# Performance work log

Measured on AMD Instinct MI355X. Metric: run time of the kernel, lower is better.

## Reference

```python
import jax, jax.numpy as jnp
import numpy as np

B, N, D = 1024, 128, 512
TEMP = 0.5          # temperature
DECAY = 0.98        # protection_decay


def setup_inputs() -> dict:
    key = jax.random.key(0)
    ks = jax.random.split(key, 16)
    s = 0.02
    return {
        "hidden": jax.random.normal(ks[0], (B, D), jnp.float32),
        "working_keys": jax.random.normal(ks[1], (B, N, D), jnp.float32),
        "working_values": jax.random.normal(ks[2], (B, N, D), jnp.float32),
        "working_protection": jax.random.uniform(ks[3], (B, N), jnp.float32),
        "working_usage": jax.random.uniform(ks[4], (B, N), jnp.float32),
        "working_age": jax.random.uniform(ks[5], (B, N), jnp.float32),
        "Wk": jax.random.normal(ks[6], (D, D), jnp.float32) * s,
        "bk": jnp.zeros((D,), jnp.float32),
        "Wv": jax.random.normal(ks[7], (D, D), jnp.float32) * s,
        "bv": jnp.zeros((D,), jnp.float32),
        "Wwr": jax.random.normal(ks[8], (D, 1), jnp.float32) * s,
        "bwr": jnp.zeros((1,), jnp.float32),
        "Wmg": jax.random.normal(ks[9], (D, 1), jnp.float32) * s,
        "bmg": jnp.zeros((1,), jnp.float32),
        "Wbd": jax.random.normal(ks[10], (D, 1), jnp.float32) * s,
        "bbd": jnp.zeros((1,), jnp.float32),
        "Wim": jax.random.normal(ks[11], (D, 1), jnp.float32) * s,
        "bim": jnp.zeros((1,), jnp.float32),
        "Woc": jax.random.normal(ks[12], (D, 1), jnp.float32) * s,
        "boc": jnp.zeros((1,), jnp.float32),
        "Wpr": jax.random.normal(ks[13], (D, 1), jnp.float32) * s,
        "bpr": jnp.zeros((1,), jnp.float32),
    }


def _normalize(x, eps=1e-6):
    # matches torch F.normalize: x / max(||x||, eps)
    n = jnp.linalg.norm(x, axis=-1, keepdims=True)
    return x / jnp.maximum(n, eps)


def reference(hidden, working_keys, working_values, working_protection,
              working_usage, working_age,
              Wk, bk, Wv, bv, Wwr, bwr, Wmg, bmg, Wbd, bbd,
              Wim, bim, Woc, boc, Wpr, bpr):
    candidate_key = jnp.tanh(hidden @ Wk + bk)              # [B,D]
    candidate_value = jnp.tanh(hidden @ Wv + bv)            # [B,D]
    write_strength = jax.nn.sigmoid(hidden @ Wwr + bwr)     # [B,1]
    importance = jax.nn.sigmoid(hidden @ Wim + bim)         # [B,1]

    norm_candidate = _normalize(candidate_key)
    norm_keys = _normalize(working_keys)
    similarity = jnp.einsum('bd,bnd->bn', norm_candidate, norm_keys)  # [B,N]

    norm_occupancy = jnp.clip(
        jnp.linalg.norm(working_values, axis=-1) / (working_values.shape[-1] ** 0.5), 0.0, 1.0)
    learned_occupancy = jax.nn.sigmoid(working_values @ Woc + boc)[..., 0]  # [B,N]
    occupancy = jnp.clip(0.5 * learned_occupancy + 0.5 * norm_occupancy, 0.0, 1.0)
    learned_protection = jax.nn.sigmoid(working_values @ Wpr + bpr)[..., 0]
    effective_protection = jnp.clip(0.4 * learned_protection + 0.6 * working_protection, 0.0, 1.0)
    effective_usage = jnp.clip(0.5 * occupancy + 0.5 * working_usage, 0.0, 1.0)
    effective_age = jnp.clip(working_age, 0.0, 1.0)

    merge_weights = jax.nn.softmax(similarity / TEMP, axis=-1)
    replace_scores = (1.15 * (1.0 - occupancy) + 0.85 * (1.0 - effective_protection)
                      + 0.65 * effective_age + 0.45 * (1.0 - effective_usage)
                      + 0.25 * (1.0 - similarity))
    replace_weights = jax.nn.softmax(replace_scores / TEMP, axis=-1)

    merge_index = jnp.argmax(merge_weights, axis=-1)      # [B]
    replace_index = jnp.argmax(replace_weights, axis=-1)  # [B]
    gi = merge_index[:, None]
    max_similarity = jnp.take_along_axis(similarity, gi, axis=1)        # [B,1]
    matched_occupancy = jnp.take_along_axis(occupancy, gi, axis=1)
    matched_usage = jnp.take_along_axis(effective_usage, gi, axis=1)
    matched_age = jnp.take_along_axis(effective_age, gi, axis=1)

    merge_preference = jax.nn.sigmoid((hidden @ Wmg + bmg) + 2.4 * max_similarity
                                      + 1.6 * (matched_occupancy - 0.5)
                                      + 1.0 * (matched_usage - 0.5)
                                      - 0.8 * matched_age)                # [B,1]
    merge_candidate = (max_similarity > 0.55) & (matched_occupancy > 0.35)  # [B,1]
    use_merge = (merge_preference >= 0.5) & merge_candidate                 # [B,1]

    target_index = jnp.where(use_merge[:, 0], merge_index, replace_index)  # [B]
    target_weights = jax.nn.one_hot(target_index, N, dtype=hidden.dtype)   # [B,N]

    binding_strength = jax.nn.sigmoid((hidden @ Wbd + bbd) + 2.2 * max_similarity)  # [B,1]
    conflict = jnp.clip(1.0 - similarity, 0.0, 1.0)
    overwrite = (0.15 + 0.85 * write_strength) * target_weights * (1.0 - 0.65 * effective_protection * conflict)  # [B,N]
    ow = overwrite[..., None]                 # [B,N,1]

    um = use_merge[:, :, None]                # [B,1,1]
    bs = binding_strength[:, :, None]         # [B,1,1]
    im = importance[:, :, None]               # [B,1,1]
    key_mix = jnp.where(um, 0.22 + 0.38 * bs, 0.78 + 0.18 * bs)
    value_mix = jnp.where(um, 0.45 + 0.35 * im, 0.75 + 0.2 * im)

    updated_keys = working_keys + ow * key_mix * (candidate_key[:, None, :] - working_keys)
    updated_values = working_values + ow * value_mix * (candidate_value[:, None, :] - working_values)

    protection_boost = overwrite * (0.5 + 0.5 * importance)
    updated_protection = jnp.clip(working_protection * DECAY + protection_boost, 0.0, 1.0)

    # stats flattened to a tuple (same order as the torch dict)
    return (updated_keys, updated_values, updated_protection,
            write_strength[:, 0], merge_preference[:, 0], binding_strength[:, 0],
            overwrite.mean(axis=-1), updated_protection.mean(axis=-1),
            max_similarity[:, 0], overwrite)
```

## Files before the change

### kernel.cpp

```cpp
#include <hip/hip_runtime.h>
#include <math.h>

#define BATCH 1024
#define NSLOT 128
#define DDIM  512
#define BB 8

__device__ __forceinline__ float sigmoidf_(float x) { return 1.0f / (1.0f + expf(-x)); }
__device__ __forceinline__ float clip01(float x) { return fminf(fmaxf(x, 0.0f), 1.0f); }
__device__ __forceinline__ float dot4(float4 a, float4 b) {
    return fmaf(a.x, b.x, fmaf(a.y, b.y, fmaf(a.z, b.z, a.w * b.w)));
}

__global__ __launch_bounds__(256) void k_gemm(
    const float* __restrict__ hidden,
    const float* __restrict__ Wk, const float* __restrict__ bk,
    const float* __restrict__ Wv, const float* __restrict__ bv,
    float* __restrict__ ck, float* __restrict__ cv)
{
    __shared__ float hs[BB][DDIM];
    const int b0 = blockIdx.x * BB;
    const int c = blockIdx.y * 256 + threadIdx.x;
    for (int i = threadIdx.x; i < BB * DDIM; i += 256)
        hs[i / DDIM][i % DDIM] = hidden[(size_t)b0 * DDIM + i];
    __syncthreads();

    float ak[BB], av[BB];
#pragma unroll
    for (int bb = 0; bb < BB; ++bb) { ak[bb] = 0.f; av[bb] = 0.f; }

#pragma unroll 4
    for (int e = 0; e < DDIM; ++e) {
        const float wk = Wk[(size_t)e * DDIM + c];
        const float wv = Wv[(size_t)e * DDIM + c];
#pragma unroll
        for (int bb = 0; bb < BB; ++bb) {
            ak[bb] = fmaf(hs[bb][e], wk, ak[bb]);
            av[bb] = fmaf(hs[bb][e], wv, av[bb]);
        }
    }
    const float bkc = bk[c], bvc = bv[c];
#pragma unroll
    for (int bb = 0; bb < BB; ++bb) {
        ck[(size_t)(b0 + bb) * DDIM + c] = tanhf(ak[bb] + bkc);
        cv[(size_t)(b0 + bb) * DDIM + c] = tanhf(av[bb] + bvc);
    }
}

__global__ __launch_bounds__(64) void k_scal(
    const float* __restrict__ hidden, const float* __restrict__ ck,
    const float* __restrict__ Wwr, const float* __restrict__ bwr,
    const float* __restrict__ Wmg, const float* __restrict__ bmg,
    const float* __restrict__ Wbd, const float* __restrict__ bbd,
    const float* __restrict__ Wim, const float* __restrict__ bim,
    float* __restrict__ scal)
{
    const int b = blockIdx.x;
    const int lane = threadIdx.x;
    const float4* h4 = (const float4*)(hidden + (size_t)b * DDIM);
    const float4* c4 = (const float4*)(ck + (size_t)b * DDIM);
    const float4* wr4 = (const float4*)Wwr;
    const float4* mg4 = (const float4*)Wmg;
    const float4* bd4 = (const float4*)Wbd;
    const float4* im4 = (const float4*)Wim;

    float dwr = 0.f, dmg = 0.f, dbd = 0.f, dim = 0.f, css = 0.f;
#pragma unroll
    for (int i = 0; i < 2; ++i) {
        const int idx = lane + i * 64;
        const float4 h = h4[idx];
        const float4 c = c4[idx];
        dwr += dot4(h, wr4[idx]);
        dmg += dot4(h, mg4[idx]);
        dbd += dot4(h, bd4[idx]);
        dim += dot4(h, im4[idx]);
        css += dot4(c, c);
    }
#pragma unroll
    for (int off = 32; off > 0; off >>= 1) {
        dwr += __shfl_down(dwr, off, 64);
        dmg += __shfl_down(dmg, off, 64);
        dbd += __shfl_down(dbd, off, 64);
        dim += __shfl_down(dim, off, 64);
        css += __shfl_down(css, off, 64);
    }
    if (lane == 0) {
        scal[b * 5 + 0] = sigmoidf_(dwr + bwr[0]);
        scal[b * 5 + 1] = sigmoidf_(dim + bim[0]);
        scal[b * 5 + 2] = dmg + bmg[0];
        scal[b * 5 + 3] = dbd + bbd[0];
        scal[b * 5 + 4] = 1.0f / fmaxf(sqrtf(css), 1e-6f);
    }
}

__global__ __launch_bounds__(256) void k_stream(
    const float* __restrict__ wkeys, const float* __restrict__ wvals,
    const float* __restrict__ wprot,
    const float* __restrict__ ck, const float* __restrict__ scal,
    const float* __restrict__ Woc, const float* __restrict__ boc,
    const float* __restrict__ Wpr, const float* __restrict__ bpr,
    float* __restrict__ out_keys, float* __restrict__ out_vals,
    float* __restrict__ sim_ws, float* __restrict__ occ_ws, float* __restrict__ epr_ws)
{
    const int wave = threadIdx.x >> 6;
    const int lane = threadIdx.x & 63;
    const size_t r = (size_t)blockIdx.x * 4 + wave;
    const int b = (int)(r >> 7);
    const float4* k4 = (const float4*)wkeys + r * (DDIM / 4);
    const float4* v4 = (const float4*)wvals + r * (DDIM / 4);
    const float4* c4 = (const float4*)ck + (size_t)b * (DDIM / 4);
    const float4* oc4 = (const float4*)Woc;
    const float4* pr4 = (const float4*)Wpr;
    float4* ok4 = (float4*)out_keys + r * (DDIM / 4);
    float4* ov4 = (float4*)out_vals + r * (DDIM / 4);

    float dk = 0.f, kk = 0.f, vv = 0.f, doc = 0.f, dpr = 0.f;
#pragma unroll
    for (int i = 0; i < 2; ++i) {
        const int idx = lane + i * 64;
        const float4 k = k4[idx];
        const float4 c = c4[idx];
        const float4 v = v4[idx];
        dk  += dot4(k, c);
        kk  += dot4(k, k);
        vv  += dot4(v, v);
        doc += dot4(v, oc4[idx]);
        dpr += dot4(v, pr4[idx]);
        ok4[idx] = k;
        ov4[idx] = v;
    }
#pragma unroll
    for (int off = 32; off > 0; off >>= 1) {
        dk  += __shfl_down(dk, off, 64);
        kk  += __shfl_down(kk, off, 64);
        vv  += __shfl_down(vv, off, 64);
        doc += __shfl_down(doc, off, 64);
        dpr += __shfl_down(dpr, off, 64);
    }
    if (lane == 0) {
        const float inv_ck = scal[b * 5 + 4];
        const float sim = dk * inv_ck * (1.0f / fmaxf(sqrtf(kk), 1e-6f));
        const float nocc = clip01(sqrtf(vv) * 0.04419417382415922f);
        const float locc = sigmoidf_(doc + boc[0]);
        const float occ = clip01(0.5f * locc + 0.5f * nocc);
        const float lpr = sigmoidf_(dpr + bpr[0]);
        const float epr = clip01(0.4f * lpr + 0.6f * wprot[r]);
        sim_ws[r] = sim;
        occ_ws[r] = occ;
        epr_ws[r] = epr;
    }
}

__global__ __launch_bounds__(128) void k_final(
    const float* __restrict__ wkeys, const float* __restrict__ wvals,
    const float* __restrict__ wprot, const float* __restrict__ wusage,
    const float* __restrict__ wage,
    const float* __restrict__ ck, const float* __restrict__ cv,
    const float* __restrict__ sim_ws, const float* __restrict__ occ_ws,
    const float* __restrict__ epr_ws, const float* __restrict__ scal,
    float* __restrict__ out_keys, float* __restrict__ out_vals,
    float* __restrict__ out_prot, float* __restrict__ out_wstr,
    float* __restrict__ out_mpref, float* __restrict__ out_bstr,
    float* __restrict__ out_ovmean, float* __restrict__ out_pmean,
    float* __restrict__ out_msim, float* __restrict__ out_ovr)
{
    const int b = blockIdx.x;
    const int n = threadIdx.x;
    __shared__ float s_sim[NSLOT], s_rs[NSLOT], s_occ[NSLOT], s_eu[NSLOT],
                     s_ea[NSLOT], s_ep[NSLOT], s_up[NSLOT];
    __shared__ int s_idx[2];

    const size_t r = (size_t)b * NSLOT + n;
    const float sim = sim_ws[r];
    const float occ = occ_ws[r];
    const float ep  = epr_ws[r];
    const float eu  = clip01(0.5f * occ + 0.5f * wusage[r]);
    const float ea  = clip01(wage[r]);
    const float rs  = 1.15f * (1.f - occ) + 0.85f * (1.f - ep) + 0.65f * ea
                    + 0.45f * (1.f - eu) + 0.25f * (1.f - sim);
    s_sim[n] = sim; s_rs[n] = rs; s_occ[n] = occ;
    s_eu[n] = eu;   s_ea[n] = ea; s_ep[n] = ep;
    __syncthreads();

    if (n == 0) {
        int mi = 0, ri = 0;
        float mv = s_sim[0], rv = s_rs[0];
        for (int i = 1; i < NSLOT; ++i) {
            if (s_sim[i] > mv) { mv = s_sim[i]; mi = i; }
            if (s_rs[i]  > rv) { rv = s_rs[i];  ri = i; }
        }
        s_idx[0] = mi; s_idx[1] = ri;
    }
    __syncthreads();

    const int mi = s_idx[0], ri = s_idx[1];
    const float max_sim = s_sim[mi];
    const float m_occ = s_occ[mi], m_eu = s_eu[mi], m_ea = s_ea[mi];
    const float wstr = scal[b * 5 + 0];
    const float imv  = scal[b * 5 + 1];
    const float mgl  = scal[b * 5 + 2];
    const float bdl  = scal[b * 5 + 3];

    const float mpref = sigmoidf_(mgl + 2.4f * max_sim + 1.6f * (m_occ - 0.5f)
                                  + 1.0f * (m_eu - 0.5f) - 0.8f * m_ea);
    const bool mcand = (max_sim > 0.55f) && (m_occ > 0.35f);
    const bool use_merge = (mpref >= 0.5f) && mcand;
    const int target = use_merge ? mi : ri;
    const float bstr = sigmoidf_(bdl + 2.2f * max_sim);

    const float conflict_t = clip01(1.f - s_sim[target]);
    const float ov = (0.15f + 0.85f * wstr) * (1.f - 0.65f * s_ep[target] * conflict_t);
    const float ovn = (n == target) ? ov : 0.f;
    out_ovr[r] = ovn;

    const float pb = ovn * (0.5f + 0.5f * imv);
    const float up = clip01(wprot[r] * 0.98f + pb);
    out_prot[r] = up;
    s_up[n] = up;
    __syncthreads();

    if (n == 0) {
        float s = 0.f;
        for (int i = 0; i < NSLOT; ++i) s += s_up[i];
        out_wstr[b]   = wstr;
        out_mpref[b]  = mpref;
        out_bstr[b]   = bstr;
        out_ovmean[b] = ov * (1.0f / NSLOT);
        out_pmean[b]  = s * (1.0f / NSLOT);
        out_msim[b]   = max_sim;
    }

    const float kmix = use_merge ? (0.22f + 0.38f * bstr) : (0.78f + 0.18f * bstr);
    const float vmix = use_merge ? (0.45f + 0.35f * imv)  : (0.75f + 0.20f * imv);
    const float fk = ov * kmix;
    const float fv = ov * vmix;
    const size_t base = ((size_t)b * NSLOT + target) * DDIM;
    const float4* wk4 = (const float4*)(wkeys + base);
    const float4* wv4 = (const float4*)(wvals + base);
    const float4* ck4 = (const float4*)(ck + (size_t)b * DDIM);
    const float4* cv4 = (const float4*)(cv + (size_t)b * DDIM);
    float4* ok4 = (float4*)(out_keys + base);
    float4* ov4 = (float4*)(out_vals + base);

    const float4 k = wk4[n], c = ck4[n];
    const float4 v = wv4[n], w = cv4[n];
    float4 nk, nv;
    nk.x = fmaf(fk, c.x - k.x, k.x); nk.y = fmaf(fk, c.y - k.y, k.y);
    nk.z = fmaf(fk, c.z - k.z, k.z); nk.w = fmaf(fk, c.w - k.w, k.w);
    nv.x = fmaf(fv, w.x - v.x, v.x); nv.y = fmaf(fv, w.y - v.y, v.y);
    nv.z = fmaf(fv, w.z - v.z, v.z); nv.w = fmaf(fv, w.w - v.w, v.w);
    ok4[n] = nk;
    ov4[n] = nv;
}

extern "C" void kernel_launch(void* const* d_in, const int* in_sizes, int n_in,
                              void* d_out, int out_size, void* d_ws, size_t ws_size,
                              hipStream_t stream)
{
    (void)in_sizes; (void)n_in; (void)out_size; (void)ws_size;

    const float* hidden = (const float*)d_in[0];
    const float* wkeys  = (const float*)d_in[1];
    const float* wvals  = (const float*)d_in[2];
    const float* wprot  = (const float*)d_in[3];
    const float* wusage = (const float*)d_in[4];
    const float* wage   = (const float*)d_in[5];
    const float* Wk  = (const float*)d_in[6];
    const float* bk  = (const float*)d_in[7];
    const float* Wv  = (const float*)d_in[8];
    const float* bv  = (const float*)d_in[9];
    const float* Wwr = (const float*)d_in[10];
    const float* bwr = (const float*)d_in[11];
    const float* Wmg = (const float*)d_in[12];
    const float* bmg = (const float*)d_in[13];
    const float* Wbd = (const float*)d_in[14];
    const float* bbd = (const float*)d_in[15];
    const float* Wim = (const float*)d_in[16];
    const float* bim = (const float*)d_in[17];
    const float* Woc = (const float*)d_in[18];
    const float* boc = (const float*)d_in[19];
    const float* Wpr = (const float*)d_in[20];
    const float* bpr = (const float*)d_in[21];

    float* out = (float*)d_out;
    const size_t BND = (size_t)BATCH * NSLOT * DDIM;
    const size_t BN  = (size_t)BATCH * NSLOT;
    float* out_keys   = out;
    float* out_vals   = out_keys + BND;
    float* out_prot   = out_vals + BND;
    float* out_wstr   = out_prot + BN;
    float* out_mpref  = out_wstr + BATCH;
    float* out_bstr   = out_mpref + BATCH;
    float* out_ovmean = out_bstr + BATCH;
    float* out_pmean  = out_ovmean + BATCH;
    float* out_msim   = out_pmean + BATCH;
    float* out_ovr    = out_msim + BATCH;

    float* ws  = (float*)d_ws;
    float* ck  = ws;
    float* cv  = ck + (size_t)BATCH * DDIM;
    float* simw = cv + (size_t)BATCH * DDIM;
    float* occw = simw + BN;
    float* eprw = occw + BN;
    float* scal = eprw + BN;

    k_gemm<<<dim3(BATCH / BB, 2), 256, 0, stream>>>(hidden, Wk, bk, Wv, bv, ck, cv);
    k_scal<<<BATCH, 64, 0, stream>>>(hidden, ck, Wwr, bwr, Wmg, bmg, Wbd, bbd,
                                     Wim, bim, scal);
    k_stream<<<(BATCH * NSLOT) / 4, 256, 0, stream>>>(
        wkeys, wvals, wprot, ck, scal, Woc, boc, Wpr, bpr,
        out_keys, out_vals, simw, occw, eprw);
    k_final<<<BATCH, NSLOT, 0, stream>>>(
        wkeys, wvals, wprot, wusage, wage, ck, cv, simw, occw, eprw, scal,
        out_keys, out_vals, out_prot, out_wstr, out_mpref, out_bstr,
        out_ovmean, out_pmean, out_msim, out_ovr);
}
```

Baseline: 1.112 ms.

## Fuse four kernels into prep and main kernels with per-batch slot streaming

Merges the GEMM and the scalar-projection kernel into one prep kernel that computes the gate dot products and candidate-key norms from the tile already in registers and shared memory. Merges the streaming similarity pass and the final selection into one per-batch kernel, which removes the sim/occ/protection workspace round-trips and two launches. Replaces the serial argmax with wave shuffle reductions. The prep kernel now uses 4 batch rows per block and 512 threads, which lowers weight reuse per block.

```diff
diff --git a/kernel.cpp b/kernel.cpp
--- a/kernel.cpp
+++ b/kernel.cpp
@@ -4,7 +4,7 @@
 #define BATCH 1024
 #define NSLOT 128
 #define DDIM  512
-#define BB 8
+#define BB 4
 
 __device__ __forceinline__ float sigmoidf_(float x) { return 1.0f / (1.0f + expf(-x)); }
 __device__ __forceinline__ float clip01(float x) { return fminf(fmaxf(x, 0.0f), 1.0f); }
@@ -12,152 +12,90 @@
     return fmaf(a.x, b.x, fmaf(a.y, b.y, fmaf(a.z, b.z, a.w * b.w)));
 }
 
-__global__ __launch_bounds__(256) void k_gemm(
+__global__ __launch_bounds__(512) void k_prep(
     const float* __restrict__ hidden,
     const float* __restrict__ Wk, const float* __restrict__ bk,
     const float* __restrict__ Wv, const float* __restrict__ bv,
-    float* __restrict__ ck, float* __restrict__ cv)
+    const float* __restrict__ Wwr, const float* __restrict__ bwr,
+    const float* __restrict__ Wmg, const float* __restrict__ bmg,
+    const float* __restrict__ Wbd, const float* __restrict__ bbd,
+    const float* __restrict__ Wim, const float* __restrict__ bim,
+    float* __restrict__ ck, float* __restrict__ cv, float* __restrict__ scal)
 {
-    __shared__ float hs[BB][DDIM];
+    __shared__ __align__(16) float hs[BB][DDIM];
+    __shared__ float sred[8][BB * 5];
     const int b0 = blockIdx.x * BB;
-    const int c = blockIdx.y * 256 + threadIdx.x;
-    for (int i = threadIdx.x; i < BB * DDIM; i += 256)
-        hs[i / DDIM][i % DDIM] = hidden[(size_t)b0 * DDIM + i];
-    __syncthreads();
-
-    float ak[BB], av[BB];
-#pragma unroll
-    for (int bb = 0; bb < BB; ++bb) { ak[bb] = 0.f; av[bb] = 0.f; }
-
+    const int c  = threadIdx.x;
+
+    {
+        const float4* h4 = (const float4*)(hidden + (size_t)b0 * DDIM);
+        ((float4*)&hs[0][0])[c] = h4[c];
+    }
+    __syncthreads();
+
+    float ak[BB] = {0.f, 0.f, 0.f, 0.f}, av[BB] = {0.f, 0.f, 0.f, 0.f};
 #pragma unroll 4
     for (int e = 0; e < DDIM; ++e) {
         const float wk = Wk[(size_t)e * DDIM + c];
         const float wv = Wv[(size_t)e * DDIM + c];
 #pragma unroll
         for (int bb = 0; bb < BB; ++bb) {
-            ak[bb] = fmaf(hs[bb][e], wk, ak[bb]);
-            av[bb] = fmaf(hs[bb][e], wv, av[bb]);
-        }
-    }
+            const float h = hs[bb][e];
+            ak[bb] = fmaf(h, wk, ak[bb]);
+            av[bb] = fmaf(h, wv, av[bb]);
+        }
+    }
+
     const float bkc = bk[c], bvc = bv[c];
+    const float wwr = Wwr[c], wmg = Wmg[c], wbd = Wbd[c], wim = Wim[c];
+    float p[BB * 5];
 #pragma unroll
     for (int bb = 0; bb < BB; ++bb) {
-        ck[(size_t)(b0 + bb) * DDIM + c] = tanhf(ak[bb] + bkc);
-        cv[(size_t)(b0 + bb) * DDIM + c] = tanhf(av[bb] + bvc);
-    }
-}
-
-__global__ __launch_bounds__(64) void k_scal(
-    const float* __restrict__ hidden, const float* __restrict__ ck,
-    const float* __restrict__ Wwr, const float* __restrict__ bwr,
-    const float* __restrict__ Wmg, const float* __restrict__ bmg,
-    const float* __restrict__ Wbd, const float* __restrict__ bbd,
-    const float* __restrict__ Wim, const float* __restrict__ bim,
-    float* __restrict__ scal)
-{
-    const int b = blockIdx.x;
-    const int lane = threadIdx.x;
-    const float4* h4 = (const float4*)(hidden + (size_t)b * DDIM);
-    const float4* c4 = (const float4*)(ck + (size_t)b * DDIM);
-    const float4* wr4 = (const float4*)Wwr;
-    const float4* mg4 = (const float4*)Wmg;
-    const float4* bd4 = (const float4*)Wbd;
-    const float4* im4 = (const float4*)Wim;
-
-    float dwr = 0.f, dmg = 0.f, dbd = 0.f, dim = 0.f, css = 0.f;
-#pragma unroll
-    for (int i = 0; i < 2; ++i) {
-        const int idx = lane + i * 64;
-        const float4 h = h4[idx];
-        const float4 c = c4[idx];
-        dwr += dot4(h, wr4[idx]);
-        dmg += dot4(h, mg4[idx]);
-        dbd += dot4(h, bd4[idx]);
-        dim += dot4(h, im4[idx]);
-        css += dot4(c, c);
-    }
-#pragma unroll
-    for (int off = 32; off > 0; off >>= 1) {
-        dwr += __shfl_down(dwr, off, 64);
-        dmg += __shfl_down(dmg, off, 64);
-        dbd += __shfl_down(dbd, off, 64);
-        dim += __shfl_down(dim, off, 64);
-        css += __shfl_down(css, off, 64);
-    }
-    if (lane == 0) {
-        scal[b * 5 + 0] = sigmoidf_(dwr + bwr[0]);
-        scal[b * 5 + 1] = sigmoidf_(dim + bim[0]);
-        scal[b * 5 + 2] = dmg + bmg[0];
-        scal[b * 5 + 3] = dbd + bbd[0];
-        scal[b * 5 + 4] = 1.0f / fmaxf(sqrtf(css), 1e-6f);
-    }
-}
-
-__global__ __launch_bounds__(256) void k_stream(
-    const float* __restrict__ wkeys, const float* __restrict__ wvals,
-    const float* __restrict__ wprot,
-    const float* __restrict__ ck, const float* __restrict__ scal,
-    const float* __restrict__ Woc, const float* __restrict__ boc,
-    const float* __restrict__ Wpr, const float* __restrict__ bpr,
-    float* __restrict__ out_keys, float* __restrict__ out_vals,
-    float* __restrict__ sim_ws, float* __restrict__ occ_ws, float* __restrict__ epr_ws)
-{
-    const int wave = threadIdx.x >> 6;
-    const int lane = threadIdx.x & 63;
-    const size_t r = (size_t)blockIdx.x * 4 + wave;
-    const int b = (int)(r >> 7);
-    const float4* k4 = (const float4*)wkeys + r * (DDIM / 4);
-    const float4* v4 = (const float4*)wvals + r * (DDIM / 4);
-    const float4* c4 = (const float4*)ck + (size_t)b * (DDIM / 4);
-    const float4* oc4 = (const float4*)Woc;
-    const float4* pr4 = (const float4*)Wpr;
-    float4* ok4 = (float4*)out_keys + r * (DDIM / 4);
-    float4* ov4 = (float4*)out_vals + r * (DDIM / 4);
-
-    float dk = 0.f, kk = 0.f, vv = 0.f, doc = 0.f, dpr = 0.f;
-#pragma unroll
-    for (int i = 0; i < 2; ++i) {
-        const int idx = lane + i * 64;
-        const float4 k = k4[idx];
-        const float4 c = c4[idx];
-        const float4 v = v4[idx];
-        dk  += dot4(k, c);
-        kk  += dot4(k, k);
-        vv  += dot4(v, v);
-        doc += dot4(v, oc4[idx]);
-        dpr += dot4(v, pr4[idx]);
-        ok4[idx] = k;
-        ov4[idx] = v;
-    }
-#pragma unroll
-    for (int off = 32; off > 0; off >>= 1) {
-        dk  += __shfl_down(dk, off, 64);
-        kk  += __shfl_down(kk, off, 64);
-        vv  += __shfl_down(vv, off, 64);
-        doc += __shfl_down(doc, off, 64);
-        dpr += __shfl_down(dpr, off, 64);
-    }
-    if (lane == 0) {
-        const float inv_ck = scal[b * 5 + 4];
-        const float sim = dk * inv_ck * (1.0f / fmaxf(sqrtf(kk), 1e-6f));
-        const float nocc = clip01(sqrtf(vv) * 0.04419417382415922f);
-        const float locc = sigmoidf_(doc + boc[0]);
-        const float occ = clip01(0.5f * locc + 0.5f * nocc);
-        const float lpr = sigmoidf_(dpr + bpr[0]);
-        const float epr = clip01(0.4f * lpr + 0.6f * wprot[r]);
-        sim_ws[r] = sim;
-        occ_ws[r] = occ;
-        epr_ws[r] = epr;
-    }
-}
-
-__global__ __launch_bounds__(128) void k_final(
+        const float k = tanhf(ak[bb] + bkc);
+        const float v = tanhf(av[bb] + bvc);
+        ck[(size_t)(b0 + bb) * DDIM + c] = k;
+        cv[(size_t)(b0 + bb) * DDIM + c] = v;
+        const float h = hs[bb][c];
+        p[bb * 5 + 0] = h * wwr;
+        p[bb * 5 + 1] = h * wim;
+        p[bb * 5 + 2] = h * wmg;
+        p[bb * 5 + 3] = h * wbd;
+        p[bb * 5 + 4] = k * k;
+    }
+#pragma unroll
+    for (int off = 32; off > 0; off >>= 1)
+#pragma unroll
+        for (int j = 0; j < BB * 5; ++j) p[j] += __shfl_down(p[j], off, 64);
+
+    const int wave = threadIdx.x >> 6, lane = threadIdx.x & 63;
+    if (lane == 0)
+#pragma unroll
+        for (int j = 0; j < BB * 5; ++j) sred[wave][j] = p[j];
+    __syncthreads();
+
+    if (threadIdx.x < BB * 5) {
+        float s = 0.f;
+#pragma unroll
+        for (int w = 0; w < 8; ++w) s += sred[w][threadIdx.x];
+        const int bb = threadIdx.x / 5, st = threadIdx.x % 5;
+        float outv;
+        if      (st == 0) outv = sigmoidf_(s + bwr[0]);
+        else if (st == 1) outv = sigmoidf_(s + bim[0]);
+        else if (st == 2) outv = s + bmg[0];
+        else if (st == 3) outv = s + bbd[0];
+        else              outv = 1.0f / fmaxf(sqrtf(s), 1e-6f);
+        scal[(b0 + bb) * 5 + st] = outv;
+    }
+}
+
+__global__ __launch_bounds__(512) void k_main(
     const float* __restrict__ wkeys, const float* __restrict__ wvals,
     const float* __restrict__ wprot, const float* __restrict__ wusage,
     const float* __restrict__ wage,
     const float* __restrict__ ck, const float* __restrict__ cv,
-    const float* __restrict__ sim_ws, const float* __restrict__ occ_ws,
-    const float* __restrict__ epr_ws, const float* __restrict__ scal,
+    const float* __restrict__ scal,
+    const float* __restrict__ Woc, const float* __restrict__ boc,
+    const float* __restrict__ Wpr, const float* __restrict__ bpr,
     float* __restrict__ out_keys, float* __restrict__ out_vals,
     float* __restrict__ out_prot, float* __restrict__ out_wstr,
     float* __restrict__ out_mpref, float* __restrict__ out_bstr,
@@ -165,92 +103,139 @@
     float* __restrict__ out_msim, float* __restrict__ out_ovr)
 {
     const int b = blockIdx.x;
-    const int n = threadIdx.x;
-    __shared__ float s_sim[NSLOT], s_rs[NSLOT], s_occ[NSLOT], s_eu[NSLOT],
-                     s_ea[NSLOT], s_ep[NSLOT], s_up[NSLOT];
+    const int wave = threadIdx.x >> 6, lane = threadIdx.x & 63;
+    const int tid = threadIdx.x;
+    __shared__ float s_sim[NSLOT], s_occ[NSLOT], s_ep[NSLOT], s_rs[NSLOT],
+                     s_eu[NSLOT], s_ea[NSLOT], s_up[NSLOT];
+    __shared__ float s_prot[NSLOT], s_usage[NSLOT], s_age[NSLOT];
     __shared__ int s_idx[2];
 
-    const size_t r = (size_t)b * NSLOT + n;
-    const float sim = sim_ws[r];
-    const float occ = occ_ws[r];
-    const float ep  = epr_ws[r];
-    const float eu  = clip01(0.5f * occ + 0.5f * wusage[r]);
-    const float ea  = clip01(wage[r]);
-    const float rs  = 1.15f * (1.f - occ) + 0.85f * (1.f - ep) + 0.65f * ea
-                    + 0.45f * (1.f - eu) + 0.25f * (1.f - sim);
-    s_sim[n] = sim; s_rs[n] = rs; s_occ[n] = occ;
-    s_eu[n] = eu;   s_ea[n] = ea; s_ep[n] = ep;
-    __syncthreads();
-
-    if (n == 0) {
-        int mi = 0, ri = 0;
-        float mv = s_sim[0], rv = s_rs[0];
-        for (int i = 1; i < NSLOT; ++i) {
-            if (s_sim[i] > mv) { mv = s_sim[i]; mi = i; }
-            if (s_rs[i]  > rv) { rv = s_rs[i];  ri = i; }
-        }
-        s_idx[0] = mi; s_idx[1] = ri;
+    const size_t rowbase = (size_t)b * NSLOT;
+    if (tid < NSLOT) {
+        s_prot[tid]  = wprot[rowbase + tid];
+        s_usage[tid] = wusage[rowbase + tid];
+        s_age[tid]   = wage[rowbase + tid];
+    }
+
+    const float4* c4  = (const float4*)(ck + (size_t)b * DDIM);
+    const float4 c0 = c4[lane],  c1 = c4[lane + 64];
+    const float4* oc4 = (const float4*)Woc;
+    const float4 o0 = oc4[lane], o1 = oc4[lane + 64];
+    const float4* pr4 = (const float4*)Wpr;
+    const float4 q0 = pr4[lane], q1 = pr4[lane + 64];
+    const float inv_ck = scal[b * 5 + 4];
+    const float boc0 = boc[0], bpr0 = bpr[0];
+    __syncthreads();
+
+    for (int i = 0; i < 16; ++i) {
+        const int n = wave * 16 + i;
+        const size_t r = rowbase + n;
+        const float4* k4 = (const float4*)wkeys + r * (DDIM / 4);
+        const float4* v4 = (const float4*)wvals + r * (DDIM / 4);
+        float4* ok4 = (float4*)out_keys + r * (DDIM / 4);
+        float4* ov4 = (float4*)out_vals + r * (DDIM / 4);
+        const float4 k0 = k4[lane], k1 = k4[lane + 64];
+        const float4 v0 = v4[lane], v1 = v4[lane + 64];
+        ok4[lane] = k0; ok4[lane + 64] = k1;
+        ov4[lane] = v0; ov4[lane + 64] = v1;
+        float dk  = dot4(k0, c0) + dot4(k1, c1);
+        float kk  = dot4(k0, k0) + dot4(k1, k1);
+        float vv  = dot4(v0, v0) + dot4(v1, v1);
+        float doc = dot4(v0, o0) + dot4(v1, o1);
+        float dpr = dot4(v0, q0) + dot4(v1, q1);
+#pragma unroll
+        for (int off = 32; off > 0; off >>= 1) {
+            dk  += __shfl_down(dk, off, 64);
+            kk  += __shfl_down(kk, off, 64);
+            vv  += __shfl_down(vv, off, 64);
+            doc += __shfl_down(doc, off, 64);
+            dpr += __shfl_down(dpr, off, 64);
+        }
+        if (lane == 0) {
+            const float sim  = dk * inv_ck * (1.0f / fmaxf(sqrtf(kk), 1e-6f));
+            const float nocc = clip01(sqrtf(vv) * 0.04419417382415922f);
+            const float occ  = clip01(0.5f * sigmoidf_(doc + boc0) + 0.5f * nocc);
+            const float ep   = clip01(0.4f * sigmoidf_(dpr + bpr0) + 0.6f * s_prot[n]);
+            const float eu   = clip01(0.5f * occ + 0.5f * s_usage[n]);
+            const float ea   = clip01(s_age[n]);
+            s_sim[n] = sim; s_occ[n] = occ; s_ep[n] = ep; s_eu[n] = eu; s_ea[n] = ea;
+            s_rs[n]  = 1.15f * (1.f - occ) + 0.85f * (1.f - ep) + 0.65f * ea
+                     + 0.45f * (1.f - eu) + 0.25f * (1.f - sim);
+        }
+    }
+    __syncthreads();
+
+    if (wave < 2) {
+        const float* arr = (wave == 0) ? s_sim : s_rs;
+        float v = arr[lane]; int idx = lane;
+        const float v2 = arr[lane + 64];
+        if (v2 > v) { v = v2; idx = lane + 64; }
+#pragma unroll
+        for (int off = 32; off > 0; off >>= 1) {
+            const float ovv = __shfl_down(v, off, 64);
+            const int   oii = __shfl_down(idx, off, 64);
+            if (ovv > v || (ovv == v && oii < idx)) { v = ovv; idx = oii; }
+        }
+        if (lane == 0) s_idx[wave] = idx;
     }
     __syncthreads();
 
     const int mi = s_idx[0], ri = s_idx[1];
     const float max_sim = s_sim[mi];
-    const float m_occ = s_occ[mi], m_eu = s_eu[mi], m_ea = s_ea[mi];
     const float wstr = scal[b * 5 + 0];
     const float imv  = scal[b * 5 + 1];
     const float mgl  = scal[b * 5 + 2];
     const float bdl  = scal[b * 5 + 3];
-
-    const float mpref = sigmoidf_(mgl + 2.4f * max_sim + 1.6f * (m_occ - 0.5f)
-                                  + 1.0f * (m_eu - 0.5f) - 0.8f * m_ea);
-    const bool mcand = (max_sim > 0.55f) && (m_occ > 0.35f);
-    const bool use_merge = (mpref >= 0.5f) && mcand;
+    const float mpref = sigmoidf_(mgl + 2.4f * max_sim + 1.6f * (s_occ[mi] - 0.5f)
+                                  + 1.0f * (s_eu[mi] - 0.5f) - 0.8f * s_ea[mi]);
+    const bool use_merge = (mpref >= 0.5f) && (max_sim > 0.55f) && (s_occ[mi] > 0.35f);
     const int target = use_merge ? mi : ri;
     const float bstr = sigmoidf_(bdl + 2.2f * max_sim);
-
     const float conflict_t = clip01(1.f - s_sim[target]);
     const float ov = (0.15f + 0.85f * wstr) * (1.f - 0.65f * s_ep[target] * conflict_t);
-    const float ovn = (n == target) ? ov : 0.f;
-    out_ovr[r] = ovn;
-
-    const float pb = ovn * (0.5f + 0.5f * imv);
-    const float up = clip01(wprot[r] * 0.98f + pb);
-    out_prot[r] = up;
-    s_up[n] = up;
-    __syncthreads();
-
-    if (n == 0) {
-        float s = 0.f;
-        for (int i = 0; i < NSLOT; ++i) s += s_up[i];
-        out_wstr[b]   = wstr;
-        out_mpref[b]  = mpref;
-        out_bstr[b]   = bstr;
-        out_ovmean[b] = ov * (1.0f / NSLOT);
-        out_pmean[b]  = s * (1.0f / NSLOT);
-        out_msim[b]   = max_sim;
-    }
-
-    const float kmix = use_merge ? (0.22f + 0.38f * bstr) : (0.78f + 0.18f * bstr);
-    const float vmix = use_merge ? (0.45f + 0.35f * imv)  : (0.75f + 0.20f * imv);
-    const float fk = ov * kmix;
-    const float fv = ov * vmix;
-    const size_t base = ((size_t)b * NSLOT + target) * DDIM;
-    const float4* wk4 = (const float4*)(wkeys + base);
-    const float4* wv4 = (const float4*)(wvals + base);
-    const float4* ck4 = (const float4*)(ck + (size_t)b * DDIM);
-    const float4* cv4 = (const float4*)(cv + (size_t)b * DDIM);
-    float4* ok4 = (float4*)(out_keys + base);
-    float4* ov4 = (float4*)(out_vals + base);
-
-    const float4 k = wk4[n], c = ck4[n];
-    const float4 v = wv4[n], w = cv4[n];
-    float4 nk, nv;
-    nk.x = fmaf(fk, c.x - k.x, k.x); nk.y = fmaf(fk, c.y - k.y, k.y);
-    nk.z = fmaf(fk, c.z - k.z, k.z); nk.w = fmaf(fk, c.w - k.w, k.w);
-    nv.x = fmaf(fv, w.x - v.x, v.x); nv.y = fmaf(fv, w.y - v.y, v.y);
-    nv.z = fmaf(fv, w.z - v.z, v.z); nv.w = fmaf(fv, w.w - v.w, v.w);
-    ok4[n] = nk;
-    ov4[n] = nv;
+
+    if (tid < NSLOT) {
+        const size_t r = rowbase + tid;
+        const float ovn = (tid == target) ? ov : 0.f;
+        out_ovr[r] = ovn;
+        const float up = clip01(s_prot[tid] * 0.98f + ovn * (0.5f + 0.5f * imv));
+        out_prot[r] = up;
+        s_up[tid] = up;
+    }
+    __syncthreads();
+
+    if (wave == 0) {
+        float s = s_up[lane] + s_up[lane + 64];
+#pragma unroll
+        for (int off = 32; off > 0; off >>= 1) s += __shfl_down(s, off, 64);
+        if (lane == 0) {
+            out_wstr[b]   = wstr;
+            out_mpref[b]  = mpref;
+            out_bstr[b]   = bstr;
+            out_ovmean[b] = ov * (1.0f / NSLOT);
+            out_pmean[b]  = s * (1.0f / NSLOT);
+            out_msim[b]   = max_sim;
+        }
+    }
+
+    if (tid < NSLOT) {
+        const float kmix = use_merge ? (0.22f + 0.38f * bstr) : (0.78f + 0.18f * bstr);
+        const float vmix = use_merge ? (0.45f + 0.35f * imv)  : (0.75f + 0.20f * imv);
+        const float fk = ov * kmix;
+        const float fv = ov * vmix;
+        const size_t base = (rowbase + target) * DDIM;
+        const float4 k = ((const float4*)(wkeys + base))[tid];
+        const float4 c = ((const float4*)(ck + (size_t)b * DDIM))[tid];
+        const float4 v = ((const float4*)(wvals + base))[tid];
+        const float4 w = ((const float4*)(cv + (size_t)b * DDIM))[tid];
+        float4 nk, nv;
+        nk.x = fmaf(fk, c.x - k.x, k.x); nk.y = fmaf(fk, c.y - k.y, k.y);
+        nk.z = fmaf(fk, c.z - k.z, k.z); nk.w = fmaf(fk, c.w - k.w, k.w);
+        nv.x = fmaf(fv, w.x - v.x, v.x); nv.y = fmaf(fv, w.y - v.y, v.y);
+        nv.z = fmaf(fv, w.z - v.z, v.z); nv.w = fmaf(fv, w.w - v.w, v.w);
+        ((float4*)(out_keys + base))[tid] = nk;
+        ((float4*)(out_vals + base))[tid] = nv;
+    }
 }
 
 extern "C" void kernel_launch(void* const* d_in, const int* in_sizes, int n_in,
@@ -296,22 +281,16 @@
     float* out_msim   = out_pmean + BATCH;
     float* out_ovr    = out_msim + BATCH;
 
-    float* ws  = (float*)d_ws;
-    float* ck  = ws;
-    float* cv  = ck + (size_t)BATCH * DDIM;
-    float* simw = cv + (size_t)BATCH * DDIM;
-    float* occw = simw + BN;
-    float* eprw = occw + BN;
-    float* scal = eprw + BN;
-
-    k_gemm<<<dim3(BATCH / BB, 2), 256, 0, stream>>>(hidden, Wk, bk, Wv, bv, ck, cv);
-    k_scal<<<BATCH, 64, 0, stream>>>(hidden, ck, Wwr, bwr, Wmg, bmg, Wbd, bbd,
-                                     Wim, bim, scal);
-    k_stream<<<(BATCH * NSLOT) / 4, 256, 0, stream>>>(
-        wkeys, wvals, wprot, ck, scal, Woc, boc, Wpr, bpr,
-        out_keys, out_vals, simw, occw, eprw);
-    k_final<<<BATCH, NSLOT, 0, stream>>>(
-        wkeys, wvals, wprot, wusage, wage, ck, cv, simw, occw, eprw, scal,
+    float* ws   = (float*)d_ws;
+    float* ck   = ws;
+    float* cv   = ck + (size_t)BATCH * DDIM;
+    float* scal = cv + (size_t)BATCH * DDIM;
+
+    k_prep<<<dim3(BATCH / BB), 512, 0, stream>>>(
+        hidden, Wk, bk, Wv, bv, Wwr, bwr, Wmg, bmg, Wbd, bbd, Wim, bim,
+        ck, cv, scal);
+    k_main<<<dim3(BATCH), 512, 0, stream>>>(
+        wkeys, wvals, wprot, wusage, wage, ck, cv, scal, Woc, boc, Wpr, bpr,
         out_keys, out_vals, out_prot, out_wstr, out_mpref, out_bstr,
         out_ovmean, out_pmean, out_msim, out_ovr);
 }
```

After: 965.9 us. 13.1% less time.
